# Performance work log

Measured on AMD Instinct MI355X. Metric: run time of the kernel, lower is better.

Reference implementation:

```python
import jax, jax.numpy as jnp
import numpy as np

B, DIM, L = 16, 512, 4096          # batch, hidden, num frames
N_FFT, HOP, WIN = 1024, 256, 1024  # STFT config (padding='same')


def setup_inputs() -> dict:
    key = jax.random.key(0)
    k1, k2, k3 = jax.random.split(key, 3)
    x = jax.random.normal(k1, (B, DIM, L), dtype=jnp.float32)
    # Conv1d(dim, 2*n_fft, kernel_size=1) weight/bias; small scale so exp(mag) stays sane
    W = jax.random.normal(k2, (2 * N_FFT, DIM), dtype=jnp.float32) * 0.02
    b = jax.random.normal(k3, (2 * N_FFT,), dtype=jnp.float32) * 0.02
    return {"x": x, "W": W, "b": b}


def reference(x, W, b):
    # 1x1 conv == channel-mixing GEMM: (B, 2*n_fft, L)
    h = jnp.einsum('bdl,od->bol', x, W) + b[None, :, None]
    mag, p = jnp.split(h, 2, axis=1)            # each (B, n_fft, L)
    mag = jnp.minimum(jnp.exp(mag), 100.0)      # exp then clip(max=100)
    S = mag * jax.lax.complex(jnp.cos(p), jnp.sin(p))
    # torch.fft.irfft(S, n_fft, dim=1): crops freq axis to n_fft//2+1 bins
    frames = jnp.fft.irfft(S, n=N_FFT, axis=1)
    # hann window, periodic=True (torch default)
    window = 0.5 * (1.0 - jnp.cos(2.0 * jnp.pi * jnp.arange(WIN, dtype=jnp.float32) / WIN))
    frames = frames * window[None, :, None]
    T = frames.shape[-1]
    out_len = (T - 1) * HOP + WIN
    idx = jnp.arange(T)[None, :] * HOP + jnp.arange(WIN)[:, None]
    y = jnp.zeros((frames.shape[0], out_len), frames.dtype).at[:, idx].add(frames)
    env = jnp.zeros((out_len,), frames.dtype).at[idx].add(
        jnp.broadcast_to((window * window)[:, None], (WIN, T)))
    pad = (WIN - HOP) // 2                      # 'same' padding trim
    return y[:, pad:out_len - pad] / env[pad:out_len - pad]
```

## Files before the change

### kernel.cpp

```cpp
#include <hip/hip_runtime.h>
#include <cstdint>
#include <cstddef>

#define BATCH  16
#define DIMK   512
#define LEN    4096
#define NFFT   1024
#define HOPS   256
#define PADT   384
#define OUTL   1048576
#define KP2    1056
#define KP2U   528
#define K2     4224

typedef __attribute__((ext_vector_type(8))) short  short8;
typedef __attribute__((ext_vector_type(4))) float  f32x4;

__device__ __forceinline__ unsigned short f2bf(float f) {
    unsigned u = __float_as_uint(f);
    u += 0x7FFFu + ((u >> 16) & 1u);
    return (unsigned short)(u >> 16);
}

__device__ __forceinline__ int clampL(int v) {
    return v < 0 ? 0 : (v > LEN - 1 ? LEN - 1 : v);
}

__device__ __forceinline__ void gld16(const unsigned short* g, unsigned short* l) {
    __builtin_amdgcn_global_load_lds(
        (const __attribute__((address_space(1))) unsigned int*)(const void*)g,
        (__attribute__((address_space(3))) unsigned int*)(void*)l, 16, 0, 0);
}

__global__ void pack_W(const float* __restrict__ W, const float* __restrict__ bvec,
                       unsigned short* __restrict__ Wb, float* __restrict__ bp) {
    const int r = blockIdx.x;
    const int i = r >> 7, j = r & 127;
    const int src = (j < 64) ? (i * 64 + j) : (1024 + i * 64 + (j - 64));
    for (int c = threadIdx.x; c < DIMK; c += 256)
        Wb[r * DIMK + c] = f2bf(W[src * DIMK + c]);
    if (threadIdx.x == 0) bp[r] = bvec[src];
}

__global__ void transpose_x(const float* __restrict__ x, unsigned short* __restrict__ xT) {
    __shared__ float tile[32][33];
    const int b = blockIdx.z;
    const int l0 = blockIdx.x * 32, d0 = blockIdx.y * 32;
    const int tx = threadIdx.x, ty = threadIdx.y;
#pragma unroll
    for (int i = 0; i < 4; ++i)
        tile[ty + 8 * i][tx] = x[((size_t)b * DIMK + d0 + ty + 8 * i) * LEN + l0 + tx];
    __syncthreads();
#pragma unroll
    for (int i = 0; i < 4; ++i)
        xT[((size_t)b * LEN + l0 + ty + 8 * i) * DIMK + d0 + tx] = f2bf(tile[tx][ty + 8 * i]);
}

__global__ void build_D(unsigned short* __restrict__ D) {
    const int idx = blockIdx.x * 256 + threadIdx.x;
    if (idx >= 256 * K2) return;
    const int srow = idx / K2;
    const int col  = idx - srow * K2;
    const int rseg = col / KP2;
    const int jj   = col - rseg * KP2;
    const int n    = srow + 256 * rseg;
    const int k    = jj >> 1;
    const float wv = 0.5f - 0.5f * __cosf((float)n * (6.283185307179586f / 1024.f));
    float v = 0.f;
    if ((jj & 1) == 0) {
        if (k == 0)        v = wv * (1.f / 1024.f);
        else if (k < 512) {
            const int p = (k * n) & 1023;
            v = 2.f * __cosf((float)p * (6.283185307179586f / 1024.f)) * wv * (1.f / 1024.f);
        } else if (k == 512) v = ((n & 1) ? -wv : wv) * (1.f / 1024.f);
    } else {
        if (k >= 1 && k < 512) {
            const int p = (k * n) & 1023;
            v = -2.f * __sinf((float)p * (6.283185307179586f / 1024.f)) * wv * (1.f / 1024.f);
        }
    }
    D[idx] = f2bf(v);
}

__global__ __launch_bounds__(256)
void gemm1_kernel(const unsigned short* __restrict__ A,
                  const unsigned short* __restrict__ Bm,
                  const float* __restrict__ bp,
                  unsigned* __restrict__ Sout)
{
    __shared__ alignas(16) char smem[17408];
    unsigned short* Alds = (unsigned short*)smem;
    unsigned short* Blds = (unsigned short*)(smem + 8192);
    unsigned*       epi  = (unsigned*)smem;

    const int tid  = threadIdx.x;
    const int lane = tid & 63, w = tid >> 6;
    const int quad = lane >> 4, ln = lane & 15;
    const int bx = blockIdx.x, by = blockIdx.y, bz = blockIdx.z;
    const int l0 = bx * 128;

    const int c0 = tid, c1 = tid + 256;
    const unsigned short* Bsrc0 = Bm + ((size_t)bz * LEN + l0 + (c0 >> 2)) * DIMK + (c0 & 3) * 8;
    const unsigned short* Bsrc1 = Bm + ((size_t)bz * LEN + l0 + (c1 >> 2)) * DIMK + (c1 & 3) * 8;

    for (int mi = 0; mi < 3; ++mi) {
        const int mt = by * 3 + mi;
        const int m0 = mt * 128;
        const int kbase = mt * 64;

        const unsigned short* Asrc0 = A + (size_t)(m0 + (c0 >> 2)) * DIMK + (c0 & 3) * 8;
        const unsigned short* Asrc1 = A + (size_t)(m0 + (c1 >> 2)) * DIMK + (c1 & 3) * 8;

        f32x4 acc[8][2];
#pragma unroll
        for (int a = 0; a < 8; ++a)
#pragma unroll
            for (int c = 0; c < 2; ++c) acc[a][c] = (f32x4){0.f, 0.f, 0.f, 0.f};

        for (int k0 = 0; k0 < DIMK; k0 += 32) {
            gld16(Asrc0 + k0, &Alds[c0 * 8]);
            gld16(Asrc1 + k0, &Alds[c1 * 8]);
            gld16(Bsrc0 + k0, &Blds[c0 * 8]);
            gld16(Bsrc1 + k0, &Blds[c1 * 8]);
            __syncthreads();

            short8 af[8], bfr[2];
#pragma unroll
            for (int rt = 0; rt < 8; ++rt)
                af[rt] = *(const short8*)&Alds[((16 * rt + ln) * 4 + quad) * 8];
#pragma unroll
            for (int ct = 0; ct < 2; ++ct)
                bfr[ct] = *(const short8*)&Blds[((32 * w + 16 * ct + ln) * 4 + quad) * 8];
#pragma unroll
            for (int rt = 0; rt < 8; ++rt)
#pragma unroll
                for (int ct = 0; ct < 2; ++ct)
                    acc[rt][ct] = __builtin_amdgcn_mfma_f32_16x16x32_bf16(af[rt], bfr[ct], acc[rt][ct], 0, 0, 0);
            __syncthreads();
        }

#pragma unroll
        for (int ct = 0; ct < 2; ++ct) {
            const int lrow = w * 16 + ln;
#pragma unroll
            for (int rt = 0; rt < 4; ++rt) {
                unsigned pk[4];
#pragma unroll
                for (int reg = 0; reg < 4; ++reg) {
                    const int rloc = 16 * rt + quad * 4 + reg;
                    const float hm = acc[rt][ct][reg]     + bp[m0 + rloc];
                    const float hp = acc[rt + 4][ct][reg] + bp[m0 + 64 + rloc];
                    const float mag = fminf(__expf(hm), 100.0f);
                    pk[reg] = (unsigned)f2bf(mag * __cosf(hp)) |
                              ((unsigned)f2bf(mag * __sinf(hp)) << 16);
                }
                *(uint4*)&epi[lrow * 68 + 16 * rt + 4 * quad] = *(uint4*)pk;
            }
            __syncthreads();
#pragma unroll
            for (int i = 0; i < 4; ++i) {
                const int c = i * 256 + tid;
                const int row = c >> 4, kc = c & 15;
                if (kbase + kc * 4 < KP2U) {
                    const int l = l0 + 32 * (row >> 4) + 16 * ct + (row & 15);
                    uint4 v = *(const uint4*)&epi[row * 68 + kc * 4];
                    *(uint4*)&Sout[((size_t)bz * LEN + l) * KP2U + kbase + kc * 4] = v;
                }
            }
            __syncthreads();
        }
    }
}

__device__ __forceinline__ float env_at(int q, int s) {
    float env = 0.f;
#pragma unroll
    for (int r = 0; r < 4; ++r) {
        const int t = q - r;
        if (t >= 0 && t < LEN) {
            const float w = 0.5f - 0.5f * __cosf((float)(s + 256 * r) * (6.283185307179586f / 1024.f));
            env += w * w;
        }
    }
    return env;
}

__global__ __launch_bounds__(256)
void gemm2_kernel(const unsigned short* __restrict__ D,
                  const unsigned short* __restrict__ Sm,
                  float* __restrict__ yout)
{
    __shared__ alignas(16) char smem[49664];
    unsigned short* Bh  = (unsigned short*)(smem + 32768);
    float*          epi = (float*)smem;

    const int tid  = threadIdx.x;
    const int lane = tid & 63, w = tid >> 6;
    const int quad = lane >> 4, ln = lane & 15;
    const int sh = w >> 1, qh = w & 1;
    const int bx = blockIdx.x, by = blockIdx.y, bz = blockIdx.z;
    const int qt0 = bx * 128, s0 = by * 128;

    unsigned short* AW = (unsigned short*)smem + w * 4096;

    const size_t srowbase = (size_t)bz * LEN;
    const int ca0 = tid, ca1 = tid + 256;
    const int c2  = 512 + (tid & 15);
    const int c2w = 512 + tid;

    const int le0 = qt0 + (ca0 >> 2) - 2;
    const int le1 = qt0 + (ca1 >> 2) - 2;
    const int le2 = qt0 + (c2  >> 2) - 2;
    const size_t ba0 = (srowbase + (size_t)clampL(le0)) * KP2 + (ca0 & 3) * 8;
    const size_t ba1 = (srowbase + (size_t)clampL(le1)) * KP2 + (ca1 & 3) * 8;
    const size_t ba2 = (srowbase + (size_t)clampL(le2)) * KP2 + (c2  & 3) * 8;
    const bool ok0 = (unsigned)le0 < (unsigned)LEN;
    const bool ok1 = (unsigned)le1 < (unsigned)LEN;
    const bool ok2 = (unsigned)le2 < (unsigned)LEN;
    const uint4 zz = {0u, 0u, 0u, 0u};

    const unsigned short* Dw = D + (size_t)(s0 + 64 * sh + (lane >> 2)) * K2 + (lane & 3) * 8;
    unsigned short* ALn = AW + lane * 8;

    auto stageA = [&](int kkel, int rseg, int buf) {
        const unsigned short* p = Dw + rseg * KP2 + kkel;
        unsigned short* l = ALn + buf * 2048;
#pragma unroll
        for (int j = 0; j < 4; ++j)
            gld16(p + (size_t)(16 * j) * K2, l + j * 512);
    };

    f32x4 acc[4][4];
#pragma unroll
    for (int a = 0; a < 4; ++a)
#pragma unroll
        for (int c = 0; c < 4; ++c) acc[a][c] = (f32x4){0.f, 0.f, 0.f, 0.f};

    auto mfmaStep = [&](int rr, int buf, int h) {
        short8 af[4], bfr[4];
#pragma unroll
        for (int rt = 0; rt < 4; ++rt)
            af[rt] = *(const short8*)&AW[buf * 2048 + (16 * rt + ln) * 32 + quad * 8];
#pragma unroll
        for (int ct = 0; ct < 4; ++ct)
            bfr[ct] = *(const short8*)&Bh[h * 4224 + ((3 - rr + 64 * qh + 16 * ct + ln) * 4 + quad) * 8];
#pragma unroll
        for (int rt = 0; rt < 4; ++rt)
#pragma unroll
            for (int ct = 0; ct < 4; ++ct)
                acc[rt][ct] = __builtin_amdgcn_mfma_f32_16x16x32_bf16(af[rt], bfr[ct], acc[rt][ct], 0, 0, 0);
    };

    uint4 v0, v1, v2;
    auto loadB = [&](int kkel) {
        v0 = *(const uint4*)&Sm[ba0 + kkel];
        v1 = *(const uint4*)&Sm[ba1 + kkel];
        v2 = *(const uint4*)&Sm[ba2 + kkel];
        if (!ok0) v0 = zz;
        if (!ok1) v1 = zz;
        if (!ok2) v2 = zz;
    };
    auto writeB = [&](int h) {
        unsigned short* Bp = Bh + h * 4224;
        *(uint4*)&Bp[ca0 * 8] = v0;
        *(uint4*)&Bp[ca1 * 8] = v1;
        if (tid < 16) *(uint4*)&Bp[c2w * 8] = v2;
    };

#define WAITVM(NSTR)                                                        \
    asm volatile("s_waitcnt vmcnt(" NSTR ")" ::: "memory");                 \
    __builtin_amdgcn_sched_barrier(0);
#define LGKM0                                                               \
    asm volatile("s_waitcnt lgkmcnt(0)" ::: "memory");                      \
    __builtin_amdgcn_sched_barrier(0);

    loadB(0);
    stageA(0, 0, 0);
    stageA(0, 1, 1);
    writeB(0);
    LGKM0
    __builtin_amdgcn_s_barrier();
    __builtin_amdgcn_sched_barrier(0);

    for (int kkIdx = 0; kkIdx < 33; ++kkIdx) {
        const int kk  = kkIdx * 32;
        const int kkn = (kkIdx < 32) ? kk + 32 : kk;
        const int h   = kkIdx & 1;

        loadB(kkn);
        WAITVM("7")
        mfmaStep(0, 0, h);
        LGKM0
        stageA(kk, 2, 0);
        WAITVM("7")
        mfmaStep(1, 1, h);
        LGKM0
        stageA(kk, 3, 1);
        WAITVM("4")
        asm volatile("" :: "v"(v0.x), "v"(v0.y), "v"(v0.z), "v"(v0.w),
                           "v"(v1.x), "v"(v1.y), "v"(v1.z), "v"(v1.w),
                           "v"(v2.x), "v"(v2.y), "v"(v2.z), "v"(v2.w));
        mfmaStep(2, 0, h);
        LGKM0
        stageA(kkn, 0, 0);
        WAITVM("4")
        mfmaStep(3, 1, h);
        LGKM0
        stageA(kkn, 1, 1);
        if (kkIdx != 32) {
            writeB(h ^ 1);
            LGKM0
            __builtin_amdgcn_s_barrier();
            __builtin_amdgcn_sched_barrier(0);
        }
    }
#undef WAITVM
#undef LGKM0

    asm volatile("s_waitcnt vmcnt(0) lgkmcnt(0)" ::: "memory");
    __syncthreads();

    float* yb = yout + (size_t)bz * OUTL;
#pragma unroll
    for (int ct = 0; ct < 4; ++ct) {
        const int qrow = qh * 16 + ln;
#pragma unroll
        for (int rt = 0; rt < 4; ++rt)
            *(f32x4*)&epi[qrow * 132 + 64 * sh + 16 * rt + 4 * quad] = acc[rt][ct];
        __syncthreads();
#pragma unroll
        for (int i = 0; i < 4; ++i) {
            const int c = i * 256 + tid;
            const int row = c >> 5, sc = c & 31;
            const int qi = qt0 + 64 * (row >> 4) + 16 * ct + (row & 15);
            const int q = qi + 1;
            const int j = 256 * qi + (s0 + sc * 4) - 128;
            if ((unsigned)j < (unsigned)(OUTL - 3)) {
                f32x4 v = *(const f32x4*)&epi[row * 132 + sc * 4];
                if (q >= 3 && q <= 4095) {
                    v *= (2.0f / 3.0f);
                } else {
#pragma unroll
                    for (int e = 0; e < 4; ++e)
                        v[e] /= env_at(q, s0 + sc * 4 + e);
                }
                *(f32x4*)&yb[j] = v;
            }
        }
        __syncthreads();
    }
}

extern "C" void kernel_launch(void* const* d_in, const int* in_sizes, int n_in,
                              void* d_out, int out_size, void* d_ws, size_t ws_size,
                              hipStream_t stream) {
    const float* x    = (const float*)d_in[0];
    const float* W    = (const float*)d_in[1];
    const float* bvec = (const float*)d_in[2];
    float* y = (float*)d_out;
    char* ws = (char*)d_ws;

    unsigned short* xT = (unsigned short*)(ws);
    unsigned short* Wb = (unsigned short*)(ws + 67108864);
    float*          bp = (float*)(ws + 68288512);
    unsigned short* D  = (unsigned short*)(ws + 68293120);
    unsigned*       S  = (unsigned*)(ws + 70455808);

    transpose_x<<<dim3(128, 16, BATCH), dim3(32, 8), 0, stream>>>(x, xT);
    pack_W<<<dim3(1152), dim3(256), 0, stream>>>(W, bvec, Wb, bp);
    build_D<<<dim3((256 * K2 + 255) / 256), dim3(256), 0, stream>>>(D);

    gemm1_kernel<<<dim3(32, 3, BATCH), dim3(256), 0, stream>>>(Wb, xT, bp, S);

    gemm2_kernel<<<dim3(33, 2, BATCH), dim3(256), 0, stream>>>(
        D, (const unsigned short*)S, y);
}
```

Baseline: 565.9 us.

## Retile gemm2 warps to 32x128 with swizzled B smem and higher occupancy

Changes the warp tiling of the second GEMM. Each warp previously computed a 64x64 tile; now each warp owns 32 rows of s and all 128 q columns. This halves the per-warp A staging and shrinks shared memory from ~49KB to ~33KB, and adds launch_bounds(256,3) so more blocks fit per CU. An XOR swizzle is added to the B tile layout in LDS to reduce bank conflicts on fragment reads. In exchange, every warp now reads all 8 B fragments per step, which raises LDS traffic, and the wait counts are retuned to match the fewer global loads.

```diff
diff --git a/kernel.cpp b/kernel.cpp
--- a/kernel.cpp
+++ b/kernel.cpp
@@ -185,23 +185,22 @@
     return env;
 }
 
-__global__ __launch_bounds__(256)
+__global__ __launch_bounds__(256, 3)
 void gemm2_kernel(const unsigned short* __restrict__ D,
                   const unsigned short* __restrict__ Sm,
                   float* __restrict__ yout)
 {
-    __shared__ alignas(16) char smem[49664];
-    unsigned short* Bh  = (unsigned short*)(smem + 32768);
+    __shared__ alignas(16) char smem[33280];
+    unsigned short* Bh  = (unsigned short*)(smem + 16384);
     float*          epi = (float*)smem;
 
     const int tid  = threadIdx.x;
     const int lane = tid & 63, w = tid >> 6;
     const int quad = lane >> 4, ln = lane & 15;
-    const int sh = w >> 1, qh = w & 1;
     const int bx = blockIdx.x, by = blockIdx.y, bz = blockIdx.z;
     const int qt0 = bx * 128, s0 = by * 128;
 
-    unsigned short* AW = (unsigned short*)smem + w * 4096;
+    unsigned short* Aw = (unsigned short*)smem + w * 2048;
 
     const size_t srowbase = (size_t)bz * LEN;
     const int ca0 = tid, ca1 = tid + 256;
@@ -219,36 +218,39 @@
     const bool ok2 = (unsigned)le2 < (unsigned)LEN;
     const uint4 zz = {0u, 0u, 0u, 0u};
 
-    const unsigned short* Dw = D + (size_t)(s0 + 64 * sh + (lane >> 2)) * K2 + (lane & 3) * 8;
-    unsigned short* ALn = AW + lane * 8;
+    const int sw0 = (ca0 * 8) ^ (((ca0 >> 2) & 7) * 8);
+    const int sw1 = (ca1 * 8) ^ (((ca1 >> 2) & 7) * 8);
+    const int sw2 = (c2w * 8) ^ (((c2w >> 2) & 7) * 8);
+
+    const unsigned short* Dw = D + (size_t)(s0 + 32 * w + (lane >> 2)) * K2 + (lane & 3) * 8;
+    unsigned short* ALn = Aw + lane * 8;
 
     auto stageA = [&](int kkel, int rseg, int buf) {
         const unsigned short* p = Dw + rseg * KP2 + kkel;
-        unsigned short* l = ALn + buf * 2048;
-#pragma unroll
-        for (int j = 0; j < 4; ++j)
-            gld16(p + (size_t)(16 * j) * K2, l + j * 512);
+        unsigned short* l = ALn + buf * 1024;
+        gld16(p, l);
+        gld16(p + (size_t)16 * K2, l + 512);
     };
 
-    f32x4 acc[4][4];
-#pragma unroll
-    for (int a = 0; a < 4; ++a)
-#pragma unroll
-        for (int c = 0; c < 4; ++c) acc[a][c] = (f32x4){0.f, 0.f, 0.f, 0.f};
+    f32x4 acc[2][8];
+#pragma unroll
+    for (int a = 0; a < 2; ++a)
+#pragma unroll
+        for (int c = 0; c < 8; ++c) acc[a][c] = (f32x4){0.f, 0.f, 0.f, 0.f};
 
     auto mfmaStep = [&](int rr, int buf, int h) {
-        short8 af[4], bfr[4];
-#pragma unroll
-        for (int rt = 0; rt < 4; ++rt)
-            af[rt] = *(const short8*)&AW[buf * 2048 + (16 * rt + ln) * 32 + quad * 8];
-#pragma unroll
-        for (int ct = 0; ct < 4; ++ct)
-            bfr[ct] = *(const short8*)&Bh[h * 4224 + ((3 - rr + 64 * qh + 16 * ct + ln) * 4 + quad) * 8];
-#pragma unroll
-        for (int rt = 0; rt < 4; ++rt)
-#pragma unroll
-            for (int ct = 0; ct < 4; ++ct)
-                acc[rt][ct] = __builtin_amdgcn_mfma_f32_16x16x32_bf16(af[rt], bfr[ct], acc[rt][ct], 0, 0, 0);
+        short8 af[2];
+#pragma unroll
+        for (int rt = 0; rt < 2; ++rt)
+            af[rt] = *(const short8*)&Aw[buf * 1024 + (16 * rt + ln) * 32 + quad * 8];
+#pragma unroll
+        for (int ct = 0; ct < 8; ++ct) {
+            const int br = 3 - rr + 16 * ct + ln;
+            const int bo = ((br * 4 + quad) * 8) ^ ((br & 7) * 8);
+            const short8 bfr = *(const short8*)&Bh[h * 4224 + bo];
+            acc[0][ct] = __builtin_amdgcn_mfma_f32_16x16x32_bf16(af[0], bfr, acc[0][ct], 0, 0, 0);
+            acc[1][ct] = __builtin_amdgcn_mfma_f32_16x16x32_bf16(af[1], bfr, acc[1][ct], 0, 0, 0);
+        }
     };
 
     uint4 v0, v1, v2;
@@ -262,9 +264,9 @@
     };
     auto writeB = [&](int h) {
         unsigned short* Bp = Bh + h * 4224;
-        *(uint4*)&Bp[ca0 * 8] = v0;
-        *(uint4*)&Bp[ca1 * 8] = v1;
-        if (tid < 16) *(uint4*)&Bp[c2w * 8] = v2;
+        *(uint4*)&Bp[sw0] = v0;
+        *(uint4*)&Bp[sw1] = v1;
+        if (tid < 16) *(uint4*)&Bp[sw2] = v2;
     };
 
 #define WAITVM(NSTR)                                                        \
@@ -288,22 +290,22 @@
         const int h   = kkIdx & 1;
 
         loadB(kkn);
-        WAITVM("7")
+        WAITVM("5")
         mfmaStep(0, 0, h);
         LGKM0
         stageA(kk, 2, 0);
-        WAITVM("7")
+        WAITVM("5")
         mfmaStep(1, 1, h);
         LGKM0
         stageA(kk, 3, 1);
-        WAITVM("4")
+        WAITVM("2")
         asm volatile("" :: "v"(v0.x), "v"(v0.y), "v"(v0.z), "v"(v0.w),
                            "v"(v1.x), "v"(v1.y), "v"(v1.z), "v"(v1.w),
                            "v"(v2.x), "v"(v2.y), "v"(v2.z), "v"(v2.w));
         mfmaStep(2, 0, h);
         LGKM0
         stageA(kkn, 0, 0);
-        WAITVM("4")
+        WAITVM("2")
         mfmaStep(3, 1, h);
         LGKM0
         stageA(kkn, 1, 1);
@@ -322,17 +324,16 @@
 
     float* yb = yout + (size_t)bz * OUTL;
 #pragma unroll
-    for (int ct = 0; ct < 4; ++ct) {
-        const int qrow = qh * 16 + ln;
-#pragma unroll
-        for (int rt = 0; rt < 4; ++rt)
-            *(f32x4*)&epi[qrow * 132 + 64 * sh + 16 * rt + 4 * quad] = acc[rt][ct];
+    for (int ct = 0; ct < 8; ++ct) {
+#pragma unroll
+        for (int rt = 0; rt < 2; ++rt)
+            *(f32x4*)&epi[ln * 132 + 32 * w + 16 * rt + 4 * quad] = acc[rt][ct];
         __syncthreads();
 #pragma unroll
-        for (int i = 0; i < 4; ++i) {
+        for (int i = 0; i < 2; ++i) {
             const int c = i * 256 + tid;
             const int row = c >> 5, sc = c & 31;
-            const int qi = qt0 + 64 * (row >> 4) + 16 * ct + (row & 15);
+            const int qi = qt0 + 16 * ct + row;
             const int q = qi + 1;
             const int j = 256 * qi + (s0 + sc * 4) - 128;
             if ((unsigned)j < (unsigned)(OUTL - 3)) {
```

Result: faster. 533.6 us (-5.7%).
